# Kernel optimization log

Hardware: AMD Instinct MI355X
Metric: run time of the kernel (lower is better)

## Reference

```python
import jax, jax.numpy as jnp
import numpy as np

B, N, IN_C, OUT_C = 32, 1024, 64, 128
ALPHA = 0.2  # LeakyReLU negative slope
NEG_INF = -1e16


def setup_inputs() -> dict:
    key = jax.random.key(0)
    k1, k2, k3, k4, k5 = jax.random.split(key, 5)
    inputs = jax.random.normal(k1, (B, N, IN_C), dtype=jnp.float32)
    # dense 0/1 adjacency mask
    graph = jax.random.randint(k2, (N, N), 0, 2).astype(jnp.float32)
    # torch nn.Linear weight layout: [out_c, in_c]
    W = jax.random.normal(k3, (OUT_C, IN_C), dtype=jnp.float32)
    b = jax.random.normal(k4, (OUT_C,), dtype=jnp.float32)
    a = jax.random.normal(k5, (2 * OUT_C, 1), dtype=jnp.float32)
    return {"inputs": inputs, "graph": graph, "W": W, "b": b, "a": a}


def reference(inputs, graph, W, b, a):
    # h = W(inputs): [B, N, D]
    h = jnp.einsum('bnt,dt->bnd', inputs, W)
    # cat([h_i, h_j]) @ a  ==  h_i @ a1 + h_j @ a2  (decomposed, no [B,N,N,2D] tensor)
    a1 = a[:OUT_C, 0]   # [D]
    a2 = a[OUT_C:, 0]   # [D]
    s1 = jnp.einsum('bnd,d->bn', h, a1)  # score contribution of node i
    s2 = jnp.einsum('bnd,d->bn', h, a2)  # score contribution of node j
    e = s1[:, :, None] + s2[:, None, :]  # [B, N, N]
    e = jnp.where(e > 0, e, ALPHA * e)   # LeakyReLU
    e = e * graph                        # zero out non-edges
    # torch masked_fill_(eq(outputs, 0), -1e16)
    e = jnp.where(e == 0.0, NEG_INF, e)
    attention = jax.nn.softmax(e, axis=2)  # [B, N, N]
    out = jnp.einsum('bij,bjd->bid', attention, h) + b  # [B, N, D]
    return out
```

## Files before the change

### kernel.cpp

```cpp
#include <hip/hip_runtime.h>
#include <hip/hip_bf16.h>

#define ALPHA 0.2f

typedef unsigned short ushort_t;
typedef unsigned int   uint_t;
typedef unsigned short ushort8 __attribute__((ext_vector_type(8)));
typedef float f32x4 __attribute__((ext_vector_type(4)));
typedef __bf16 bf16x8 __attribute__((ext_vector_type(8)));

__device__ __forceinline__ ushort_t f2bf(float f) {
  unsigned u = __float_as_uint(f);
  u += 0x7fffu + ((u >> 16) & 1u);
  return (ushort_t)(u >> 16);
}
__device__ __forceinline__ float bf2f(ushort_t b) {
  return __uint_as_float((unsigned)b << 16);
}

__global__ __launch_bounds__(128) void gat_u_kernel(
    const float* __restrict__ W, const float* __restrict__ avec,
    float* __restrict__ u)
{
  const int t  = threadIdx.x;
  const int k  = t & 63;
  const int ao = (t >> 6) * 128;
  float a0 = 0.f, a1 = 0.f, a2 = 0.f, a3 = 0.f;
  for (int d = 0; d < 128; d += 4) {
    a0 = fmaf(avec[ao + d + 0], W[(d + 0) * 64 + k], a0);
    a1 = fmaf(avec[ao + d + 1], W[(d + 1) * 64 + k], a1);
    a2 = fmaf(avec[ao + d + 2], W[(d + 2) * 64 + k], a2);
    a3 = fmaf(avec[ao + d + 3], W[(d + 3) * 64 + k], a3);
  }
  u[t] = (a0 + a1) + (a2 + a3);
}

__global__ __launch_bounds__(256) void gat_pack_kernel(
    const float* __restrict__ graph, uint_t* __restrict__ gmask)
{
  const int row = blockIdx.x, t = threadIdx.x;
  __shared__ uint_t nibs[256];
  float4 g = ((const float4*)(graph + (size_t)row * 1024))[t];
  uint_t nib = (g.x != 0.f ? 1u : 0u) | (g.y != 0.f ? 2u : 0u) |
               (g.z != 0.f ? 4u : 0u) | (g.w != 0.f ? 8u : 0u);
  nibs[t] = nib;
  __syncthreads();
  if (t < 32) {
    uint_t w = 0;
#pragma unroll
    for (int k = 0; k < 8; ++k) w |= nibs[t * 8 + k] << (4 * k);
    gmask[(size_t)row * 32 + t] = w;
  }
}

__global__ __launch_bounds__(256) void gat_h_kernel(
    const float* __restrict__ inp, const float* __restrict__ W,
    const float* __restrict__ uvec, ushort_t* __restrict__ hT,
    float* __restrict__ s1, float* __restrict__ s2)
{
  const int b  = blockIdx.x >> 4;
  const int n0 = (blockIdx.x & 15) << 6;
  const int t  = threadIdx.x;
  const int d  = t & 127;
  const int nh = t >> 7;

  __shared__ float    x_lds[64][68];
  __shared__ float    u_lds[128];
  __shared__ ushort_t h_tile[128][72];

  float wreg[64];
  {
    const float4* wrow = (const float4*)(W + d * 64);
#pragma unroll
    for (int k = 0; k < 16; ++k) {
      float4 v = wrow[k];
      wreg[4*k+0] = v.x; wreg[4*k+1] = v.y; wreg[4*k+2] = v.z; wreg[4*k+3] = v.w;
    }
  }
  if (t < 128) u_lds[t] = uvec[t];

  {
    const float4* xsrc = (const float4*)(inp + ((size_t)b * 1024 + n0) * 64);
#pragma unroll
    for (int k = 0; k < 4; ++k) {
      const int g = k * 256 + t;
      const int n = g >> 4, c = g & 15;
      *(float4*)&x_lds[n][c * 4] = xsrc[g];
    }
  }
  __syncthreads();

  for (int r = 0; r < 32; ++r) {
    const int n = nh * 32 + r;
    const float* xr = &x_lds[n][0];
    float ax = 0.f, ay = 0.f, az = 0.f, aw = 0.f;
#pragma unroll
    for (int k = 0; k < 16; ++k) {
      float4 xv = *(const float4*)&xr[4 * k];
      ax = fmaf(wreg[4*k+0], xv.x, ax);
      ay = fmaf(wreg[4*k+1], xv.y, ay);
      az = fmaf(wreg[4*k+2], xv.z, az);
      aw = fmaf(wreg[4*k+3], xv.w, aw);
    }
    h_tile[d][n] = f2bf((ax + ay) + (az + aw));
  }

  if (t < 128) {
    const int n = t & 63, which = t >> 6;
    const float* xr = &x_lds[n][0];
    const float* uu = &u_lds[which * 64];
    float a0 = 0.f, a1 = 0.f, a2 = 0.f, a3 = 0.f;
#pragma unroll
    for (int k = 0; k < 16; ++k) {
      float4 xv = *(const float4*)&xr[4 * k];
      a0 = fmaf(xv.x, uu[4*k+0], a0);
      a1 = fmaf(xv.y, uu[4*k+1], a1);
      a2 = fmaf(xv.z, uu[4*k+2], a2);
      a3 = fmaf(xv.w, uu[4*k+3], a3);
    }
    const float sv = (a0 + a1) + (a2 + a3);
    if (which == 0) s1[(size_t)b * 1024 + n0 + n] = sv;
    else            s2[(size_t)b * 1024 + n0 + n] = sv;
  }
  __syncthreads();

#pragma unroll
  for (int it = 0; it < 4; ++it) {
    const int d2 = it * 32 + (t >> 3);
    const int ch = (t & 7) * 8;
    ushort8 v = *(const ushort8*)&h_tile[d2][ch];
    *(ushort8*)(hT + ((size_t)b * 128 + d2) * 1024 + n0 + ch) = v;
  }
}

__global__ __launch_bounds__(256) void gat_attn_kernel(
    const uint_t* __restrict__ gmask, const ushort_t* __restrict__ hT,
    const float* __restrict__ s1g, const float* __restrict__ s2g,
    const float* __restrict__ bias, float* __restrict__ out)
{
  const int ic = blockIdx.x;
  const int b  = blockIdx.y;
  const int i0 = ic << 5;
  const int t  = threadIdx.x;
  const int w  = t >> 6;
  const int l  = t & 63;

  __shared__ float    s2_lds[1024];
  __shared__ uint_t   mask_lds[32][33];
  __shared__ ushort_t p_lds[32][72];
  __shared__ ushort_t ht_lds[128][72];
  __shared__ float    red_part[32][8];
  __shared__ float    red_row[32];

  {
    const float4* src = (const float4*)(s2g + (size_t)b * 1024);
    ((float4*)s2_lds)[t] = src[t];
  }
  {
    const uint4 mv = ((const uint4*)(gmask + (size_t)(i0 + (t >> 3)) * 32))[t & 7];
    const int mr = t >> 3, mc = (t & 7) * 4;
    mask_lds[mr][mc + 0] = mv.x; mask_lds[mr][mc + 1] = mv.y;
    mask_lds[mr][mc + 2] = mv.z; mask_lds[mr][mc + 3] = mv.w;
  }
  const int irow = t >> 3;
  const int jsl  = (t & 7) * 8;
  const int bo   = (t & 3) * 8;
  const int widx = (t >> 2) & 1;
  const float s1v = s1g[(size_t)b * 1024 + i0 + irow];
  const ushort_t* htb = hT + (size_t)b * 128 * 1024;
  __syncthreads();

  float mx_local = -1e30f;
  for (int jt = 0; jt < 16; ++jt) {
    const int j0 = jt * 64;
    const uint_t word = mask_lds[irow][jt * 2 + widx];
    float4 sA = *(const float4*)(s2_lds + j0 + jsl);
    float4 sB = *(const float4*)(s2_lds + j0 + jsl + 4);
    if ((word >> (bo + 0)) & 1u) mx_local = fmaxf(mx_local, sA.x);
    if ((word >> (bo + 1)) & 1u) mx_local = fmaxf(mx_local, sA.y);
    if ((word >> (bo + 2)) & 1u) mx_local = fmaxf(mx_local, sA.z);
    if ((word >> (bo + 3)) & 1u) mx_local = fmaxf(mx_local, sA.w);
    if ((word >> (bo + 4)) & 1u) mx_local = fmaxf(mx_local, sB.x);
    if ((word >> (bo + 5)) & 1u) mx_local = fmaxf(mx_local, sB.y);
    if ((word >> (bo + 6)) & 1u) mx_local = fmaxf(mx_local, sB.z);
    if ((word >> (bo + 7)) & 1u) mx_local = fmaxf(mx_local, sB.w);
  }
  red_part[irow][t & 7] = mx_local;
  __syncthreads();
  if (t < 32) {
    float m = red_part[t][0];
#pragma unroll
    for (int k = 1; k < 8; ++k) m = fmaxf(m, red_part[t][k]);
    red_row[t] = m;
  }
  __syncthreads();
  const float tm = s1v + red_row[irow];
  const float Mi = tm > 0.f ? tm : ALPHA * tm;
  __syncthreads();

  float den_local = 0.f;
  f32x4 c[2][2];
#pragma unroll
  for (int is = 0; is < 2; ++is)
#pragma unroll
    for (int ds = 0; ds < 2; ++ds)
      c[is][ds] = f32x4{0.f, 0.f, 0.f, 0.f};

  for (int jt = 0; jt < 16; ++jt) {
    const int j0 = jt * 64;
    ushort8 hv[4];
#pragma unroll
    for (int k = 0; k < 4; ++k) {
      const int c2 = t + k * 256;
      const int dd = c2 >> 3;
      const int jc = (c2 & 7) * 8;
      hv[k] = *(const ushort8*)(htb + (size_t)dd * 1024 + j0 + jc);
    }
    const uint_t word = mask_lds[irow][jt * 2 + widx];
    float4 sA = *(const float4*)(s2_lds + j0 + jsl);
    float4 sB = *(const float4*)(s2_lds + j0 + jsl + 4);
    float ss[8] = {sA.x, sA.y, sA.z, sA.w, sB.x, sB.y, sB.z, sB.w};
    ushort8 pb;
#pragma unroll
    for (int e = 0; e < 8; ++e) {
      float te = s1v + ss[e];
      float v  = te > 0.f ? te : ALPHA * te;
      float p = (((word >> (bo + e)) & 1u) && v != 0.f) ? __expf(v - Mi) : 0.f;
      pb[e] = f2bf(p);
      den_local += bf2f(pb[e]);
    }
    *(ushort8*)&p_lds[irow][jsl] = pb;
#pragma unroll
    for (int k = 0; k < 4; ++k) {
      const int c2 = t + k * 256;
      const int dd = c2 >> 3;
      const int jc = (c2 & 7) * 8;
      *(ushort8*)&ht_lds[dd][jc] = hv[k];
    }
    __syncthreads();
#pragma unroll
    for (int kk = 0; kk < 2; ++kk) {
      const int kcol = kk * 32 + (l >> 4) * 8;
      bf16x8 av[2];
#pragma unroll
      for (int is = 0; is < 2; ++is)
        av[is] = __builtin_bit_cast(
            bf16x8, *(const ushort8*)&p_lds[is * 16 + (l & 15)][kcol]);
#pragma unroll
      for (int ds = 0; ds < 2; ++ds) {
        bf16x8 bv = __builtin_bit_cast(
            bf16x8,
            *(const ushort8*)&ht_lds[w * 32 + ds * 16 + (l & 15)][kcol]);
#pragma unroll
        for (int is = 0; is < 2; ++is)
          c[is][ds] = __builtin_amdgcn_mfma_f32_16x16x32_bf16(
              av[is], bv, c[is][ds], 0, 0, 0);
      }
    }
    __syncthreads();
  }

  red_part[irow][t & 7] = den_local;
  __syncthreads();
  if (t < 32) {
    float s = red_part[t][0];
#pragma unroll
    for (int k = 1; k < 8; ++k) s += red_part[t][k];
    red_row[t] = s;
  }
  __syncthreads();

#pragma unroll
  for (int ds = 0; ds < 2; ++ds) {
    const int col = w * 32 + ds * 16 + (l & 15);
    const float bc = bias[col];
#pragma unroll
    for (int is = 0; is < 2; ++is) {
#pragma unroll
      for (int r = 0; r < 4; ++r) {
        const int row = is * 16 + (l >> 4) * 4 + r;
        const float dr = red_row[row];
        const float val = dr > 0.f ? c[is][ds][r] / dr + bc : bc;
        out[((size_t)b * 1024 + i0 + row) * 128 + col] = val;
      }
    }
  }
}

extern "C" void kernel_launch(void* const* d_in, const int* in_sizes, int n_in,
                              void* d_out, int out_size, void* d_ws, size_t ws_size,
                              hipStream_t stream) {
  (void)in_sizes; (void)n_in; (void)out_size; (void)ws_size;
  const float* inp   = (const float*)d_in[0];
  const float* graph = (const float*)d_in[1];
  const float* W     = (const float*)d_in[2];
  const float* bias  = (const float*)d_in[3];
  const float* avec  = (const float*)d_in[4];
  float* out = (float*)d_out;

  char* ws = (char*)d_ws;
  ushort_t* hT = (ushort_t*)ws;
  float* s1    = (float*)(ws + (size_t)8 * 1024 * 1024);
  float* s2    = s1 + 32 * 1024;
  float* u     = s2 + 32 * 1024;
  uint_t* gm   = (uint_t*)(ws + (size_t)8 * 1024 * 1024 + 512 * 1024);

  gat_pack_kernel<<<1024, 256, 0, stream>>>(graph, gm);
  gat_u_kernel<<<1, 128, 0, stream>>>(W, avec, u);
  gat_h_kernel<<<512, 256, 0, stream>>>(inp, W, u, hT, s1, s2);
  gat_attn_kernel<<<dim3(32, 32), 256, 0, stream>>>(gm, hT, s1, s2, bias, out);
}
```

Baseline: 68.37 us.

## Double-buffer attention j-tiles with prefetch and fold u computation into pack kernel

The attention kernel's j-loop now uses 32-wide tiles with double-buffered LDS for probabilities and hT. The next tile's global loads and its softmax staging overlap the current tile's MFMAs, which halves the barriers per tile and raises MFMA priority with setprio. The separate one-block u kernel is merged into block 0 of the mask-pack kernel to save a launch. In exchange, the loop runs twice as many smaller iterations, and block 0 of the pack kernel does extra serial work.

```diff
diff --git a/kernel.cpp b/kernel.cpp
--- a/kernel.cpp
+++ b/kernel.cpp
@@ -6,6 +6,7 @@
 typedef unsigned short ushort_t;
 typedef unsigned int   uint_t;
 typedef unsigned short ushort8 __attribute__((ext_vector_type(8)));
+typedef unsigned short ushortv4 __attribute__((ext_vector_type(4)));
 typedef float f32x4 __attribute__((ext_vector_type(4)));
 typedef __bf16 bf16x8 __attribute__((ext_vector_type(8)));
 
@@ -18,25 +19,10 @@
   return __uint_as_float((unsigned)b << 16);
 }
 
-__global__ __launch_bounds__(128) void gat_u_kernel(
-    const float* __restrict__ W, const float* __restrict__ avec,
+__global__ __launch_bounds__(256) void gat_pack_kernel(
+    const float* __restrict__ graph, const float* __restrict__ W,
+    const float* __restrict__ avec, uint_t* __restrict__ gmask,
     float* __restrict__ u)
-{
-  const int t  = threadIdx.x;
-  const int k  = t & 63;
-  const int ao = (t >> 6) * 128;
-  float a0 = 0.f, a1 = 0.f, a2 = 0.f, a3 = 0.f;
-  for (int d = 0; d < 128; d += 4) {
-    a0 = fmaf(avec[ao + d + 0], W[(d + 0) * 64 + k], a0);
-    a1 = fmaf(avec[ao + d + 1], W[(d + 1) * 64 + k], a1);
-    a2 = fmaf(avec[ao + d + 2], W[(d + 2) * 64 + k], a2);
-    a3 = fmaf(avec[ao + d + 3], W[(d + 3) * 64 + k], a3);
-  }
-  u[t] = (a0 + a1) + (a2 + a3);
-}
-
-__global__ __launch_bounds__(256) void gat_pack_kernel(
-    const float* __restrict__ graph, uint_t* __restrict__ gmask)
 {
   const int row = blockIdx.x, t = threadIdx.x;
   __shared__ uint_t nibs[256];
@@ -46,10 +32,22 @@
   nibs[t] = nib;
   __syncthreads();
   if (t < 32) {
-    uint_t w = 0;
-#pragma unroll
-    for (int k = 0; k < 8; ++k) w |= nibs[t * 8 + k] << (4 * k);
-    gmask[(size_t)row * 32 + t] = w;
+    uint_t wd = 0;
+#pragma unroll
+    for (int k = 0; k < 8; ++k) wd |= nibs[t * 8 + k] << (4 * k);
+    gmask[(size_t)row * 32 + t] = wd;
+  }
+  if (row == 0 && t < 128) {
+    const int k  = t & 63;
+    const int ao = (t >> 6) * 128;
+    float a0 = 0.f, a1 = 0.f, a2 = 0.f, a3 = 0.f;
+    for (int d = 0; d < 128; d += 4) {
+      a0 = fmaf(avec[ao + d + 0], W[(d + 0) * 64 + k], a0);
+      a1 = fmaf(avec[ao + d + 1], W[(d + 1) * 64 + k], a1);
+      a2 = fmaf(avec[ao + d + 2], W[(d + 2) * 64 + k], a2);
+      a3 = fmaf(avec[ao + d + 3], W[(d + 3) * 64 + k], a3);
+    }
+    u[t] = (a0 + a1) + (a2 + a3);
   }
 }
 
@@ -147,8 +145,8 @@
 
   __shared__ float    s2_lds[1024];
   __shared__ uint_t   mask_lds[32][33];
-  __shared__ ushort_t p_lds[32][72];
-  __shared__ ushort_t ht_lds[128][72];
+  __shared__ ushort_t p_lds[2][32][40];
+  __shared__ ushort_t ht_lds[2][128][40];
   __shared__ float    red_part[32][8];
   __shared__ float    red_row[32];
 
@@ -163,27 +161,21 @@
     mask_lds[mr][mc + 2] = mv.z; mask_lds[mr][mc + 3] = mv.w;
   }
   const int irow = t >> 3;
-  const int jsl  = (t & 7) * 8;
-  const int bo   = (t & 3) * 8;
-  const int widx = (t >> 2) & 1;
+  const int jsl  = (t & 7) * 4;
+  const int sr   = t >> 2;
+  const int sc   = (t & 3) * 8;
   const float s1v = s1g[(size_t)b * 1024 + i0 + irow];
   const ushort_t* htb = hT + (size_t)b * 128 * 1024;
   __syncthreads();
 
   float mx_local = -1e30f;
-  for (int jt = 0; jt < 16; ++jt) {
-    const int j0 = jt * 64;
-    const uint_t word = mask_lds[irow][jt * 2 + widx];
-    float4 sA = *(const float4*)(s2_lds + j0 + jsl);
-    float4 sB = *(const float4*)(s2_lds + j0 + jsl + 4);
-    if ((word >> (bo + 0)) & 1u) mx_local = fmaxf(mx_local, sA.x);
-    if ((word >> (bo + 1)) & 1u) mx_local = fmaxf(mx_local, sA.y);
-    if ((word >> (bo + 2)) & 1u) mx_local = fmaxf(mx_local, sA.z);
-    if ((word >> (bo + 3)) & 1u) mx_local = fmaxf(mx_local, sA.w);
-    if ((word >> (bo + 4)) & 1u) mx_local = fmaxf(mx_local, sB.x);
-    if ((word >> (bo + 5)) & 1u) mx_local = fmaxf(mx_local, sB.y);
-    if ((word >> (bo + 6)) & 1u) mx_local = fmaxf(mx_local, sB.z);
-    if ((word >> (bo + 7)) & 1u) mx_local = fmaxf(mx_local, sB.w);
+  for (int jt = 0; jt < 32; ++jt) {
+    const uint_t word = mask_lds[irow][jt];
+    float4 sA = *(const float4*)(s2_lds + jt * 32 + jsl);
+    if ((word >> (jsl + 0)) & 1u) mx_local = fmaxf(mx_local, sA.x);
+    if ((word >> (jsl + 1)) & 1u) mx_local = fmaxf(mx_local, sA.y);
+    if ((word >> (jsl + 2)) & 1u) mx_local = fmaxf(mx_local, sA.z);
+    if ((word >> (jsl + 3)) & 1u) mx_local = fmaxf(mx_local, sA.w);
   }
   red_part[irow][t & 7] = mx_local;
   __syncthreads();
@@ -196,7 +188,6 @@
   __syncthreads();
   const float tm = s1v + red_row[irow];
   const float Mi = tm > 0.f ? tm : ALPHA * tm;
-  __syncthreads();
 
   float den_local = 0.f;
   f32x4 c[2][2];
@@ -206,58 +197,63 @@
     for (int ds = 0; ds < 2; ++ds)
       c[is][ds] = f32x4{0.f, 0.f, 0.f, 0.f};
 
-  for (int jt = 0; jt < 16; ++jt) {
-    const int j0 = jt * 64;
-    ushort8 hv[4];
-#pragma unroll
-    for (int k = 0; k < 4; ++k) {
-      const int c2 = t + k * 256;
-      const int dd = c2 >> 3;
-      const int jc = (c2 & 7) * 8;
-      hv[k] = *(const ushort8*)(htb + (size_t)dd * 1024 + j0 + jc);
-    }
-    const uint_t word = mask_lds[irow][jt * 2 + widx];
-    float4 sA = *(const float4*)(s2_lds + j0 + jsl);
-    float4 sB = *(const float4*)(s2_lds + j0 + jsl + 4);
-    float ss[8] = {sA.x, sA.y, sA.z, sA.w, sB.x, sB.y, sB.z, sB.w};
-    ushort8 pb;
-#pragma unroll
-    for (int e = 0; e < 8; ++e) {
-      float te = s1v + ss[e];
-      float v  = te > 0.f ? te : ALPHA * te;
-      float p = (((word >> (bo + e)) & 1u) && v != 0.f) ? __expf(v - Mi) : 0.f;
-      pb[e] = f2bf(p);
-      den_local += bf2f(pb[e]);
-    }
-    *(ushort8*)&p_lds[irow][jsl] = pb;
-#pragma unroll
-    for (int k = 0; k < 4; ++k) {
-      const int c2 = t + k * 256;
-      const int dd = c2 >> 3;
-      const int jc = (c2 & 7) * 8;
-      *(ushort8*)&ht_lds[dd][jc] = hv[k];
-    }
+#define STAGE_COMPUTE(nj, bi, hva, hvb)                                      \
+  {                                                                          \
+    const uint_t word = mask_lds[irow][nj];                                  \
+    const float4 sA = *(const float4*)(s2_lds + (nj) * 32 + jsl);            \
+    const float ss[4] = {sA.x, sA.y, sA.z, sA.w};                            \
+    ushortv4 pb;                                                             \
+    _Pragma("unroll")                                                        \
+    for (int e = 0; e < 4; ++e) {                                            \
+      float te = s1v + ss[e];                                                \
+      float v  = te > 0.f ? te : ALPHA * te;                                 \
+      float p  = (((word >> (jsl + e)) & 1u) && v != 0.f)                    \
+                     ? __expf(v - Mi) : 0.f;                                 \
+      pb[e] = f2bf(p);                                                       \
+      den_local += bf2f(pb[e]);                                              \
+    }                                                                        \
+    *(ushortv4*)&p_lds[bi][irow][jsl] = pb;                                  \
+    *(ushort8*)&ht_lds[bi][sr][sc] = (hva);                                  \
+    *(ushort8*)&ht_lds[bi][sr + 64][sc] = (hvb);                             \
+  }
+
+#define DO_MFMA(bi)                                                          \
+  {                                                                          \
+    bf16x8 av0 = __builtin_bit_cast(bf16x8,                                  \
+        *(const ushort8*)&p_lds[bi][(l & 15)][(l >> 4) * 8]);                \
+    bf16x8 av1 = __builtin_bit_cast(bf16x8,                                  \
+        *(const ushort8*)&p_lds[bi][16 + (l & 15)][(l >> 4) * 8]);           \
+    bf16x8 bv0 = __builtin_bit_cast(bf16x8,                                  \
+        *(const ushort8*)&ht_lds[bi][w * 32 + (l & 15)][(l >> 4) * 8]);      \
+    bf16x8 bv1 = __builtin_bit_cast(bf16x8,                                  \
+        *(const ushort8*)&ht_lds[bi][w * 32 + 16 + (l & 15)][(l >> 4) * 8]); \
+    c[0][0] = __builtin_amdgcn_mfma_f32_16x16x32_bf16(av0, bv0, c[0][0], 0, 0, 0); \
+    c[1][0] = __builtin_amdgcn_mfma_f32_16x16x32_bf16(av1, bv0, c[1][0], 0, 0, 0); \
+    c[0][1] = __builtin_amdgcn_mfma_f32_16x16x32_bf16(av0, bv1, c[0][1], 0, 0, 0); \
+    c[1][1] = __builtin_amdgcn_mfma_f32_16x16x32_bf16(av1, bv1, c[1][1], 0, 0, 0); \
+  }
+
+  {
+    ushort8 hva = *(const ushort8*)(htb + (size_t)sr * 1024 + sc);
+    ushort8 hvb = *(const ushort8*)(htb + (size_t)(sr + 64) * 1024 + sc);
+    STAGE_COMPUTE(0, 0, hva, hvb);
+  }
+  __syncthreads();
+
+  int cur = 0;
+  for (int jt = 0; jt < 32; ++jt) {
+    ushort8 nha, nhb;
+    const int nj = jt + 1;
+    if (nj < 32) {
+      nha = *(const ushort8*)(htb + (size_t)sr * 1024 + nj * 32 + sc);
+      nhb = *(const ushort8*)(htb + (size_t)(sr + 64) * 1024 + nj * 32 + sc);
+    }
+    __builtin_amdgcn_s_setprio(1);
+    DO_MFMA(cur);
+    __builtin_amdgcn_s_setprio(0);
+    if (nj < 32) STAGE_COMPUTE(nj, cur ^ 1, nha, nhb);
     __syncthreads();
-#pragma unroll
-    for (int kk = 0; kk < 2; ++kk) {
-      const int kcol = kk * 32 + (l >> 4) * 8;
-      bf16x8 av[2];
-#pragma unroll
-      for (int is = 0; is < 2; ++is)
-        av[is] = __builtin_bit_cast(
-            bf16x8, *(const ushort8*)&p_lds[is * 16 + (l & 15)][kcol]);
-#pragma unroll
-      for (int ds = 0; ds < 2; ++ds) {
-        bf16x8 bv = __builtin_bit_cast(
-            bf16x8,
-            *(const ushort8*)&ht_lds[w * 32 + ds * 16 + (l & 15)][kcol]);
-#pragma unroll
-        for (int is = 0; is < 2; ++is)
-          c[is][ds] = __builtin_amdgcn_mfma_f32_16x16x32_bf16(
-              av[is], bv, c[is][ds], 0, 0, 0);
-      }
-    }
-    __syncthreads();
+    cur ^= 1;
   }
 
   red_part[irow][t & 7] = den_local;
@@ -305,8 +301,7 @@
   float* u     = s2 + 32 * 1024;
   uint_t* gm   = (uint_t*)(ws + (size_t)8 * 1024 * 1024 + 512 * 1024);
 
-  gat_pack_kernel<<<1024, 256, 0, stream>>>(graph, gm);
-  gat_u_kernel<<<1, 128, 0, stream>>>(W, avec, u);
+  gat_pack_kernel<<<1024, 256, 0, stream>>>(graph, W, avec, gm, u);
   gat_h_kernel<<<512, 256, 0, stream>>>(inp, W, u, hT, s1, s2);
   gat_attn_kernel<<<dim3(32, 32), 256, 0, stream>>>(gm, hT, s1, s2, bias, out);
 }
```

New measurement: 67.39 us. Within noise of the previous version (-1.4%).
